# Optimization experiments

Measured on AMD Instinct MI355X. Metric: run time of the kernel, lower is better.

## Reference

```python
import jax, jax.numpy as jnp
import numpy as np

# Dimensions: B point clouds of S points each, C channels, H heads of dim D
B, S, C, H, D = 8, 2048, 128, 4, 32
EPS = 1e-5  # GroupNorm eps (torch default)


def setup_inputs() -> dict:
    key = jax.random.key(0)
    ks = jax.random.split(key, 3)
    x = jax.random.normal(ks[0], (B, S, C), dtype=jnp.float32)
    # GroupNorm(num_groups=1) affine params (per-channel)
    gamma = jnp.ones((C,), dtype=jnp.float32)
    beta = jnp.zeros((C,), dtype=jnp.float32)
    # to_qkv: 1x1 Minkowski conv == linear, no bias; output = 3*H*D channels
    w_qkv = jax.random.normal(ks[1], (3 * H * D, C), dtype=jnp.float32) * 0.02
    # to_out: 1x1 conv with bias, H*D -> C
    w_out = jax.random.normal(ks[2], (C, H * D), dtype=jnp.float32) * 0.02
    b_out = jnp.zeros((C,), dtype=jnp.float32)
    return {"x": x, "gamma": gamma, "beta": beta, "w_qkv": w_qkv,
            "w_out": w_out, "b_out": b_out}


def reference(x, gamma, beta, w_qkv, w_out, b_out):
    scale = D ** -0.5
    # GroupNorm(num_groups=1) applied per cloud over ALL channels and points
    mu = jnp.mean(x, axis=(1, 2), keepdims=True)
    var = jnp.var(x, axis=(1, 2), keepdims=True)
    nx = (x - mu) * jax.lax.rsqrt(var + EPS) * gamma + beta  # [B,S,C]
    # Pointwise qkv projection (no bias)
    qkv = jnp.einsum('bsc,fc->bsf', nx, w_qkv)  # [B,S,3*H*D]
    q, k, v = jnp.split(qkv, 3, axis=-1)
    q = q.reshape(B, S, H, D) * scale
    k = k.reshape(B, S, H, D)
    v = v.reshape(B, S, H, D)
    # Per-cloud multi-head self-attention (block-diagonal over clouds)
    attn = jax.nn.softmax(jnp.einsum('bihd,bjhd->bhij', q, k), axis=-1)  # [B,H,S,S]
    o = jnp.einsum('bhij,bjhd->bihd', attn, v).reshape(B, S, H * D)
    # Output projection (with bias) + residual
    return jnp.einsum('bsf,cf->bsc', o, w_out) + b_out + x
```

## Files before the change

### kernel.cpp

```cpp
#include <hip/hip_runtime.h>
#include <hip/hip_bf16.h>

#define B_ 8
#define S_ 2048
#define C_ 128
#define H_ 4
#define D_ 32
#define SC_ (S_*C_)
#define HD_ (H_*D_)

typedef short bf16x8 __attribute__((ext_vector_type(8)));
typedef float f32x4 __attribute__((ext_vector_type(4)));
union FragU { uint4 u; bf16x8 h; };

__device__ __forceinline__ unsigned short f2bf(float f) {
  __hip_bfloat16 h = __float2bfloat16(f);
  return *reinterpret_cast<unsigned short*>(&h);
}
__device__ __forceinline__ unsigned int pk2t(float a, float b) {
  union { float f; unsigned int u; } ua, ub;
  ua.f = a; ub.f = b;
  return __builtin_amdgcn_perm(ub.u, ua.u, 0x07060302u);
}
__device__ __forceinline__ unsigned int pk2r(float a, float b) {
  return (unsigned int)f2bf(a) | ((unsigned int)f2bf(b) << 16);
}
#define EXP2(x) __builtin_amdgcn_exp2f(x)

__global__ __launch_bounds__(256) void k_stats1(const float* __restrict__ x,
                                                const float* __restrict__ wqkv,
                                                const float* __restrict__ wout,
                                                float* __restrict__ part,
                                                unsigned short* __restrict__ wq_bf,
                                                unsigned short* __restrict__ wo_bf) {
  __shared__ float ssum[256], ssq[256];
  int b = blockIdx.x >> 5, sl = blockIdx.x & 31;
  int tid = threadIdx.x;
  int gid = blockIdx.x * 256 + tid;
  if (gid < 16384) {
    int e = gid * 4;
    const float4 u = (e < 49152) ? *(const float4*)(wqkv + e) : *(const float4*)(wout + e - 49152);
    unsigned short tv[4] = {f2bf(u.x), f2bf(u.y), f2bf(u.z), f2bf(u.w)};
    unsigned short* dst = (e < 49152) ? (wq_bf + e) : (wo_bf + e - 49152);
    *(uint2*)dst = *(uint2*)tv;
  }
  const float4* xp = (const float4*)(x + (size_t)b * SC_);
  float sum = 0.f, sq = 0.f;
  for (int i = sl * 2048 + tid; i < (sl + 1) * 2048; i += 256) {
    float4 u = xp[i];
    sum += u.x + u.y + u.z + u.w;
    sq  += u.x*u.x + u.y*u.y + u.z*u.z + u.w*u.w;
  }
  ssum[tid] = sum; ssq[tid] = sq;
  __syncthreads();
  for (int s = 128; s > 0; s >>= 1) {
    if (tid < s) { ssum[tid] += ssum[tid + s]; ssq[tid] += ssq[tid + s]; }
    __syncthreads();
  }
  if (tid == 0) { part[blockIdx.x * 2] = ssum[0]; part[blockIdx.x * 2 + 1] = ssq[0]; }
}

__global__ __launch_bounds__(512) void k_qkv(const float* __restrict__ x,
                                             const float* __restrict__ gamma,
                                             const float* __restrict__ beta,
                                             const unsigned short* __restrict__ wq_bf,
                                             const float* __restrict__ part,
                                             unsigned short* __restrict__ q_ws,
                                             unsigned short* __restrict__ k_ws,
                                             unsigned short* __restrict__ v_ws) {
  __shared__ __align__(16) unsigned short Nls[32][136];
  __shared__ float gs[128], bs[128];
  __shared__ float st2[2];
  const int tid = threadIdx.x;
  const int w = tid >> 6, l = tid & 63, g = l >> 4, i = l & 15;
  const int gr0 = blockIdx.x * 32;
  const int b = gr0 >> 11;
  if (tid < 128) { gs[tid] = gamma[tid]; bs[tid] = beta[tid]; }
  if (tid < 32) {
    float s1 = part[(b * 32 + tid) * 2];
    float s2 = part[(b * 32 + tid) * 2 + 1];
    #pragma unroll
    for (int m = 16; m >= 1; m >>= 1) { s1 += __shfl_xor(s1, m); s2 += __shfl_xor(s2, m); }
    if (tid == 0) {
      float mu = s1 / (float)SC_;
      float var = s2 / (float)SC_ - mu * mu;
      st2[0] = mu; st2[1] = rsqrtf(var + 1e-5f);
    }
  }
  __syncthreads();
  const float mu = st2[0], rstd = st2[1];
  {
    const float4* xp = (const float4*)(x + (size_t)gr0 * C_);
    #pragma unroll
    for (int t = 0; t < 2; ++t) {
      int e = tid + t * 512;
      float4 u = xp[e];
      int r = e >> 5, c0 = (e & 31) * 4;
      float4 gv = *(const float4*)&gs[c0];
      float4 bv = *(const float4*)&bs[c0];
      unsigned short tv[4] = {
        f2bf((u.x - mu) * rstd * gv.x + bv.x),
        f2bf((u.y - mu) * rstd * gv.y + bv.y),
        f2bf((u.z - mu) * rstd * gv.z + bv.z),
        f2bf((u.w - mu) * rstd * gv.w + bv.w)};
      *(uint2*)&Nls[r][c0] = *(uint2*)tv;
    }
  }
  __syncthreads();
  f32x4 acc[2][3];
  #pragma unroll
  for (int rt = 0; rt < 2; ++rt)
    #pragma unroll
    for (int n = 0; n < 3; ++n) acc[rt][n] = (f32x4){0.f,0.f,0.f,0.f};

  #pragma unroll
  for (int kk = 0; kk < 4; ++kk) {
    FragU bfr[3];
    #pragma unroll
    for (int n = 0; n < 3; ++n)
      bfr[n].u = *(const uint4*)(wq_bf + (size_t)((w * 3 + n) * 16 + i) * 128 + kk * 32 + 8 * g);
    FragU af[2];
    #pragma unroll
    for (int rt = 0; rt < 2; ++rt) af[rt].u = *(const uint4*)&Nls[rt * 16 + i][kk * 32 + 8 * g];
    #pragma unroll
    for (int n = 0; n < 3; ++n)
      #pragma unroll
      for (int rt = 0; rt < 2; ++rt)
        acc[rt][n] = __builtin_amdgcn_mfma_f32_16x16x32_bf16(af[rt].h, bfr[n].h, acc[rt][n], 0, 0, 0);
  }
  __syncthreads();
  unsigned short (*Vbuf)[32] = (unsigned short(*)[32])&Nls[0][0];

  const float SCQ = 0.17677669529663687f * 1.4426950408889634f;
  const int base64 = ((blockIdx.x & 63) >> 1) * 64;
  const int odd32 = (blockIdx.x & 1) * 32;
  #pragma unroll
  for (int n = 0; n < 3; ++n) {
    int f = (w * 3 + n) * 16 + i;
    int which = f >> 7, fi = f & 127, h = fi >> 5, dd = fi & 31;
    #pragma unroll
    for (int rt = 0; rt < 2; ++rt) {
      if (which == 2) {
        *(unsigned int*)&Vbuf[fi][8 * g + 4 * rt]     = pk2r(acc[rt][n][0], acc[rt][n][1]);
        *(unsigned int*)&Vbuf[fi][8 * g + 4 * rt + 2] = pk2r(acc[rt][n][2], acc[rt][n][3]);
      } else {
        #pragma unroll
        for (int r = 0; r < 4; ++r) {
          int s = (gr0 + rt * 16 + 4 * g + r) & (S_ - 1);
          if (which == 0) {
            q_ws[(((size_t)b * H_ + h) * S_ + s) * D_ + dd] = f2bf(acc[rt][n][r] * SCQ);
          } else {
            k_ws[(((size_t)b * H_ + h) * S_ + s) * D_ + dd] = f2bf(acc[rt][n][r]);
          }
        }
      }
    }
  }
  __syncthreads();
  {
    int fi = tid >> 2, ch = tid & 3;
    int h = fi >> 5, dd = fi & 31;
    uint4 vv = *(const uint4*)&Vbuf[fi][ch * 8];
    *(uint4*)(v_ws + (((size_t)b * H_ + h) * D_ + dd) * S_ + base64 + odd32 + ch * 8) = vv;
  }
}

__global__ __launch_bounds__(256) void k_attn(const unsigned short* __restrict__ qg,
                                              const unsigned short* __restrict__ kg,
                                              const unsigned short* __restrict__ vg,
                                              unsigned short* __restrict__ og) {
  __shared__ __align__(16) unsigned short Kls[2][128][40];
  __shared__ __align__(16) unsigned short Vt[2][32][136];
  const int tid = threadIdx.x;
  const int w = tid >> 6, l = tid & 63;
  const int g = l >> 4, i = l & 15;
  const int qb = blockIdx.x, h = blockIdx.y, b = blockIdx.z;
  const size_t base = ((size_t)b * H_ + h) * (size_t)(S_ * D_);

  FragU qf;
  qf.u = *(const uint4*)(qg + base + (size_t)(qb * 64 + w * 16 + i) * D_ + 8 * g);
  FragU onef;
  onef.u = (uint4){0x3F803F80u, 0x3F803F80u, 0x3F803F80u, 0x3F803F80u};

  const int kr0 = tid >> 2, kc = tid & 3;
  const int vr0 = tid >> 4, vc = tid & 15;
  const uint4* kp = (const uint4*)(kg + base);
  const unsigned short* vt = vg + base;

  f32x4 oac[2] = {{0.f,0.f,0.f,0.f},{0.f,0.f,0.f,0.f}};
  f32x4 sac = {0.f,0.f,0.f,0.f};

  *(uint4*)&Kls[0][kr0][kc * 8]      = kp[kr0 * 4 + kc];
  *(uint4*)&Kls[0][kr0 + 64][kc * 8] = kp[(kr0 + 64) * 4 + kc];
  *(uint4*)&Vt[0][vr0][vc * 8]       = *(const uint4*)(vt + (size_t)vr0 * S_ + vc * 8);
  *(uint4*)&Vt[0][vr0 + 16][vc * 8]  = *(const uint4*)(vt + (size_t)(vr0 + 16) * S_ + vc * 8);

  for (int kt = 0; kt < 16; ++kt) {
    const int cur = kt & 1;
    __syncthreads();
    uint4 nk0, nk1, nv0, nv1;
    const bool pf = kt < 15;
    if (pf) {
      nk0 = kp[((kt + 1) * 128 + kr0) * 4 + kc];
      nk1 = kp[((kt + 1) * 128 + kr0 + 64) * 4 + kc];
      nv0 = *(const uint4*)(vt + (size_t)vr0 * S_ + (kt + 1) * 128 + vc * 8);
      nv1 = *(const uint4*)(vt + (size_t)(vr0 + 16) * S_ + (kt + 1) * 128 + vc * 8);
    }
    #pragma unroll
    for (int sub = 0; sub < 2; ++sub) {
      f32x4 sf[4];
      __builtin_amdgcn_s_setprio(1);
      #pragma unroll
      for (int n = 0; n < 4; ++n) {
        FragU kf; kf.u = *(const uint4*)&Kls[cur][sub * 64 + n * 16 + i][8 * g];
        f32x4 z = {0.f, 0.f, 0.f, 0.f};
        sf[n] = __builtin_amdgcn_mfma_f32_16x16x32_bf16(kf.h, qf.h, z, 0, 0, 0);
      }
      __builtin_amdgcn_s_setprio(0);
      FragU pa0, pa1;
      pa0.u = (uint4){pk2t(EXP2(sf[0][0]), EXP2(sf[0][1])),
                      pk2t(EXP2(sf[0][2]), EXP2(sf[0][3])),
                      pk2t(EXP2(sf[1][0]), EXP2(sf[1][1])),
                      pk2t(EXP2(sf[1][2]), EXP2(sf[1][3]))};
      pa1.u = (uint4){pk2t(EXP2(sf[2][0]), EXP2(sf[2][1])),
                      pk2t(EXP2(sf[2][2]), EXP2(sf[2][3])),
                      pk2t(EXP2(sf[3][0]), EXP2(sf[3][1])),
                      pk2t(EXP2(sf[3][2]), EXP2(sf[3][3]))};
      __builtin_amdgcn_s_setprio(1);
      sac = __builtin_amdgcn_mfma_f32_16x16x32_bf16(pa0.h, onef.h, sac, 0, 0, 0);
      #pragma unroll
      for (int n = 0; n < 2; ++n) {
        FragU vf; vf.u = *(const uint4*)&Vt[cur][n * 16 + i][sub * 64 + 8 * g];
        oac[n] = __builtin_amdgcn_mfma_f32_16x16x32_bf16(pa0.h, vf.h, oac[n], 0, 0, 0);
      }
      sac = __builtin_amdgcn_mfma_f32_16x16x32_bf16(pa1.h, onef.h, sac, 0, 0, 0);
      #pragma unroll
      for (int n = 0; n < 2; ++n) {
        FragU vf; vf.u = *(const uint4*)&Vt[cur][n * 16 + i][sub * 64 + 32 + 8 * g];
        oac[n] = __builtin_amdgcn_mfma_f32_16x16x32_bf16(pa1.h, vf.h, oac[n], 0, 0, 0);
      }
      __builtin_amdgcn_s_setprio(0);
    }
    if (pf) {
      *(uint4*)&Kls[cur ^ 1][kr0][kc * 8]      = nk0;
      *(uint4*)&Kls[cur ^ 1][kr0 + 64][kc * 8] = nk1;
      *(uint4*)&Vt[cur ^ 1][vr0][vc * 8]       = nv0;
      *(uint4*)&Vt[cur ^ 1][vr0 + 16][vc * 8]  = nv1;
    }
  }
  #pragma unroll
  for (int n = 0; n < 2; ++n) {
    #pragma unroll
    for (int r = 0; r < 4; ++r) {
      size_t row = (size_t)qb * 64 + w * 16 + 4 * g + r;
      og[((size_t)b * S_ + row) * HD_ + h * D_ + n * 16 + i] = f2bf(oac[n][r] / sac[r]);
    }
  }
}

__global__ __launch_bounds__(512) void k_out(const unsigned short* __restrict__ o,
                                             const unsigned short* __restrict__ wo_bf,
                                             const float* __restrict__ bo,
                                             const float* __restrict__ x,
                                             float* __restrict__ out) {
  const int tid = threadIdx.x;
  const int w = tid >> 6, l = tid & 63, g = l >> 4, i = l & 15;
  const int gr0 = blockIdx.x * 32;
  const int c = w * 16 + i;
  f32x4 acc[2] = {{0,0,0,0},{0,0,0,0}};
  #pragma unroll
  for (int kk = 0; kk < 4; ++kk) {
    FragU bfr;
    bfr.u = *(const uint4*)(wo_bf + (size_t)c * HD_ + kk * 32 + 8 * g);
    #pragma unroll
    for (int rt = 0; rt < 2; ++rt) {
      FragU af;
      af.u = *(const uint4*)(o + (size_t)(gr0 + rt * 16 + i) * HD_ + kk * 32 + 8 * g);
      acc[rt] = __builtin_amdgcn_mfma_f32_16x16x32_bf16(af.h, bfr.h, acc[rt], 0, 0, 0);
    }
  }
  float bias = bo[c];
  #pragma unroll
  for (int rt = 0; rt < 2; ++rt) {
    #pragma unroll
    for (int r = 0; r < 4; ++r) {
      size_t idx = (size_t)(gr0 + rt * 16 + 4 * g + r) * C_ + c;
      out[idx] = acc[rt][r] + bias + x[idx];
    }
  }
}

extern "C" void kernel_launch(void* const* d_in, const int* in_sizes, int n_in,
                              void* d_out, int out_size, void* d_ws, size_t ws_size,
                              hipStream_t stream) {
  const float* x     = (const float*)d_in[0];
  const float* gamma = (const float*)d_in[1];
  const float* beta  = (const float*)d_in[2];
  const float* wqkv  = (const float*)d_in[3];
  const float* wout  = (const float*)d_in[4];
  const float* bout  = (const float*)d_in[5];
  float* out = (float*)d_out;

  float* part  = (float*)((char*)d_ws + 64);
  unsigned short* wq_bf = (unsigned short*)((char*)d_ws + 4096);
  unsigned short* wo_bf = wq_bf + 49152;
  unsigned short* q_ws = (unsigned short*)((char*)d_ws + 4096 + 98304 + 32768);
  const size_t per = (size_t)B_ * H_ * S_ * D_;
  unsigned short* k_ws = q_ws + per;
  unsigned short* v_ws = k_ws + per;
  unsigned short* o_ws = v_ws + per;

  hipLaunchKernelGGL(k_stats1, dim3(256), dim3(256), 0, stream, x, wqkv, wout, part, wq_bf, wo_bf);
  hipLaunchKernelGGL(k_qkv, dim3(512), dim3(512), 0, stream,
                     x, gamma, beta, wq_bf, part, q_ws, k_ws, v_ws);
  hipLaunchKernelGGL(k_attn, dim3(S_ / 64, H_, B_), dim3(256), 0, stream,
                     q_ws, k_ws, v_ws, o_ws);
  hipLaunchKernelGGL(k_out, dim3(512), dim3(512), 0, stream,
                     o_ws, wo_bf, bout, x, out);
}
```

Measured before the change: 59.17 us.

## Process two query tiles per wave and remap attention grid for XCD locality

```diff
diff --git a/kernel.cpp b/kernel.cpp
--- a/kernel.cpp
+++ b/kernel.cpp
@@ -174,11 +174,17 @@
   const int tid = threadIdx.x;
   const int w = tid >> 6, l = tid & 63;
   const int g = l >> 4, i = l & 15;
-  const int qb = blockIdx.x, h = blockIdx.y, b = blockIdx.z;
+  const int bid = blockIdx.x;
+  const int wid = (bid & 7) * 64 + (bid >> 3);
+  const int qb = wid & 15;
+  const int hb = wid >> 4;
+  const int h = hb & 3, b = hb >> 2;
   const size_t base = ((size_t)b * H_ + h) * (size_t)(S_ * D_);
 
-  FragU qf;
-  qf.u = *(const uint4*)(qg + base + (size_t)(qb * 64 + w * 16 + i) * D_ + 8 * g);
+  FragU qf[2];
+  #pragma unroll
+  for (int qt = 0; qt < 2; ++qt)
+    qf[qt].u = *(const uint4*)(qg + base + (size_t)(qb * 128 + w * 32 + qt * 16 + i) * D_ + 8 * g);
   FragU onef;
   onef.u = (uint4){0x3F803F80u, 0x3F803F80u, 0x3F803F80u, 0x3F803F80u};
 
@@ -187,8 +193,9 @@
   const uint4* kp = (const uint4*)(kg + base);
   const unsigned short* vt = vg + base;
 
-  f32x4 oac[2] = {{0.f,0.f,0.f,0.f},{0.f,0.f,0.f,0.f}};
-  f32x4 sac = {0.f,0.f,0.f,0.f};
+  f32x4 oac[2][2] = {{{0.f,0.f,0.f,0.f},{0.f,0.f,0.f,0.f}},
+                     {{0.f,0.f,0.f,0.f},{0.f,0.f,0.f,0.f}}};
+  f32x4 sac[2] = {{0.f,0.f,0.f,0.f},{0.f,0.f,0.f,0.f}};
 
   *(uint4*)&Kls[0][kr0][kc * 8]      = kp[kr0 * 4 + kc];
   *(uint4*)&Kls[0][kr0 + 64][kc * 8] = kp[(kr0 + 64) * 4 + kc];
@@ -208,38 +215,42 @@
     }
     #pragma unroll
     for (int sub = 0; sub < 2; ++sub) {
-      f32x4 sf[4];
-      __builtin_amdgcn_s_setprio(1);
-      #pragma unroll
-      for (int n = 0; n < 4; ++n) {
-        FragU kf; kf.u = *(const uint4*)&Kls[cur][sub * 64 + n * 16 + i][8 * g];
-        f32x4 z = {0.f, 0.f, 0.f, 0.f};
-        sf[n] = __builtin_amdgcn_mfma_f32_16x16x32_bf16(kf.h, qf.h, z, 0, 0, 0);
+      FragU kf[4], vf[4];
+      #pragma unroll
+      for (int n = 0; n < 4; ++n) kf[n].u = *(const uint4*)&Kls[cur][sub * 64 + n * 16 + i][8 * g];
+      #pragma unroll
+      for (int n = 0; n < 2; ++n) {
+        vf[n].u     = *(const uint4*)&Vt[cur][n * 16 + i][sub * 64 + 8 * g];
+        vf[2 + n].u = *(const uint4*)&Vt[cur][n * 16 + i][sub * 64 + 32 + 8 * g];
       }
-      __builtin_amdgcn_s_setprio(0);
-      FragU pa0, pa1;
-      pa0.u = (uint4){pk2t(EXP2(sf[0][0]), EXP2(sf[0][1])),
-                      pk2t(EXP2(sf[0][2]), EXP2(sf[0][3])),
-                      pk2t(EXP2(sf[1][0]), EXP2(sf[1][1])),
-                      pk2t(EXP2(sf[1][2]), EXP2(sf[1][3]))};
-      pa1.u = (uint4){pk2t(EXP2(sf[2][0]), EXP2(sf[2][1])),
-                      pk2t(EXP2(sf[2][2]), EXP2(sf[2][3])),
-                      pk2t(EXP2(sf[3][0]), EXP2(sf[3][1])),
-                      pk2t(EXP2(sf[3][2]), EXP2(sf[3][3]))};
-      __builtin_amdgcn_s_setprio(1);
-      sac = __builtin_amdgcn_mfma_f32_16x16x32_bf16(pa0.h, onef.h, sac, 0, 0, 0);
-      #pragma unroll
-      for (int n = 0; n < 2; ++n) {
-        FragU vf; vf.u = *(const uint4*)&Vt[cur][n * 16 + i][sub * 64 + 8 * g];
-        oac[n] = __builtin_amdgcn_mfma_f32_16x16x32_bf16(pa0.h, vf.h, oac[n], 0, 0, 0);
+      #pragma unroll
+      for (int qt = 0; qt < 2; ++qt) {
+        f32x4 sf[4];
+        __builtin_amdgcn_s_setprio(1);
+        #pragma unroll
+        for (int n = 0; n < 4; ++n) {
+          f32x4 z = {0.f, 0.f, 0.f, 0.f};
+          sf[n] = __builtin_amdgcn_mfma_f32_16x16x32_bf16(kf[n].h, qf[qt].h, z, 0, 0, 0);
+        }
+        __builtin_amdgcn_s_setprio(0);
+        FragU pa0, pa1;
+        pa0.u = (uint4){pk2t(EXP2(sf[0][0]), EXP2(sf[0][1])),
+                        pk2t(EXP2(sf[0][2]), EXP2(sf[0][3])),
+                        pk2t(EXP2(sf[1][0]), EXP2(sf[1][1])),
+                        pk2t(EXP2(sf[1][2]), EXP2(sf[1][3]))};
+        pa1.u = (uint4){pk2t(EXP2(sf[2][0]), EXP2(sf[2][1])),
+                        pk2t(EXP2(sf[2][2]), EXP2(sf[2][3])),
+                        pk2t(EXP2(sf[3][0]), EXP2(sf[3][1])),
+                        pk2t(EXP2(sf[3][2]), EXP2(sf[3][3]))};
+        __builtin_amdgcn_s_setprio(1);
+        sac[qt] = __builtin_amdgcn_mfma_f32_16x16x32_bf16(pa0.h, onef.h, sac[qt], 0, 0, 0);
+        oac[qt][0] = __builtin_amdgcn_mfma_f32_16x16x32_bf16(pa0.h, vf[0].h, oac[qt][0], 0, 0, 0);
+        oac[qt][1] = __builtin_amdgcn_mfma_f32_16x16x32_bf16(pa0.h, vf[1].h, oac[qt][1], 0, 0, 0);
+        sac[qt] = __builtin_amdgcn_mfma_f32_16x16x32_bf16(pa1.h, onef.h, sac[qt], 0, 0, 0);
+        oac[qt][0] = __builtin_amdgcn_mfma_f32_16x16x32_bf16(pa1.h, vf[2].h, oac[qt][0], 0, 0, 0);
+        oac[qt][1] = __builtin_amdgcn_mfma_f32_16x16x32_bf16(pa1.h, vf[3].h, oac[qt][1], 0, 0, 0);
+        __builtin_amdgcn_s_setprio(0);
       }
-      sac = __builtin_amdgcn_mfma_f32_16x16x32_bf16(pa1.h, onef.h, sac, 0, 0, 0);
-      #pragma unroll
-      for (int n = 0; n < 2; ++n) {
-        FragU vf; vf.u = *(const uint4*)&Vt[cur][n * 16 + i][sub * 64 + 32 + 8 * g];
-        oac[n] = __builtin_amdgcn_mfma_f32_16x16x32_bf16(pa1.h, vf.h, oac[n], 0, 0, 0);
-      }
-      __builtin_amdgcn_s_setprio(0);
     }
     if (pf) {
       *(uint4*)&Kls[cur ^ 1][kr0][kc * 8]      = nk0;
@@ -249,11 +260,14 @@
     }
   }
   #pragma unroll
-  for (int n = 0; n < 2; ++n) {
-    #pragma unroll
-    for (int r = 0; r < 4; ++r) {
-      size_t row = (size_t)qb * 64 + w * 16 + 4 * g + r;
-      og[((size_t)b * S_ + row) * HD_ + h * D_ + n * 16 + i] = f2bf(oac[n][r] / sac[r]);
+  for (int qt = 0; qt < 2; ++qt) {
+    #pragma unroll
+    for (int n = 0; n < 2; ++n) {
+      #pragma unroll
+      for (int r = 0; r < 4; ++r) {
+        size_t row = (size_t)qb * 128 + w * 32 + qt * 16 + 4 * g + r;
+        og[((size_t)b * S_ + row) * HD_ + h * D_ + n * 16 + i] = f2bf(oac[qt][n][r] / sac[qt][r]);
+      }
     }
   }
 }
@@ -313,7 +327,7 @@
   hipLaunchKernelGGL(k_stats1, dim3(256), dim3(256), 0, stream, x, wqkv, wout, part, wq_bf, wo_bf);
   hipLaunchKernelGGL(k_qkv, dim3(512), dim3(512), 0, stream,
                      x, gamma, beta, wq_bf, part, q_ws, k_ws, v_ws);
-  hipLaunchKernelGGL(k_attn, dim3(S_ / 64, H_, B_), dim3(256), 0, stream,
+  hipLaunchKernelGGL(k_attn, dim3(512), dim3(256), 0, stream,
                      q_ws, k_ws, v_ws, o_ws);
   hipLaunchKernelGGL(k_out, dim3(512), dim3(512), 0, stream,
                      o_ws, wo_bf, bout, x, out);
```

Result: slower. 61.65 us (+4.2%).
